# Kernel tuning notes

Hardware: AMD Instinct MI355X
Metric: run time of the kernel (lower is better)

The kernel has to match this reference:

```python
import jax, jax.numpy as jnp
import numpy as np

N = 100_000   # nodes
E = 1_600_000 # edges (avg degree 16)
D = 64        # in_channel == out_channel (residual requires equality)
EPS = 1e-5    # BatchNorm1d eps


def setup_inputs() -> dict:
    key = jax.random.key(0)
    ks = jax.random.split(key, 8)
    x = jax.random.normal(ks[0], (N, D), dtype=jnp.float32)
    adj_val = jax.random.uniform(ks[1], (E,), dtype=jnp.float32) * 0.25  # sparse poly_adj values
    W = jax.random.normal(ks[2], (D, D), dtype=jnp.float32) / np.sqrt(D)  # Linear weight [out,in]
    b = jnp.zeros((D,), dtype=jnp.float32)
    gamma = jnp.ones((D,), dtype=jnp.float32)
    beta = jnp.zeros((D,), dtype=jnp.float32)
    adj_row = jax.random.randint(ks[3], (E,), 0, N, dtype=jnp.int32)
    adj_col = jax.random.randint(ks[4], (E,), 0, N, dtype=jnp.int32)
    return {"x": x, "adj_val": adj_val, "W": W, "b": b,
            "gamma": gamma, "beta": beta, "adj_row": adj_row, "adj_col": adj_col}


def reference(x, adj_val, W, b, gamma, beta, adj_row, adj_col):
    # h = poly_adj @ x  (COO SpMM via gather + segment_sum)
    h = jax.ops.segment_sum(adj_val[:, None] * x[adj_col], adj_row, num_segments=N)
    # Linear
    h = h @ W.T + b
    # residual
    h = h + x
    # BatchNorm1d (training-mode batch stats, biased variance)
    mean = jnp.mean(h, axis=0)
    var = jnp.mean(jnp.square(h - mean), axis=0)
    h = (h - mean) * jax.lax.rsqrt(var + EPS) * gamma + beta
    # ReLU (dropout with p=0 is identity)
    h = jax.nn.relu(h)
    return h
```

## Files before the change

### kernel.cpp

```cpp
#include <hip/hip_runtime.h>

#define DCH 64
#define BN_EPS 1e-5f

#define SUPSH 12
#define NSUPMAX 32
#define CAPS 67584
#define CHA 2048
#define CHB 2048
#define CPS 33
#define FPS 128
#define CAPF 704
#define CITER 8
#define SITER 3

__device__ __forceinline__ unsigned bf16pair(float lo, float hi) {
    unsigned ul = (__float_as_uint(lo) + 0x8000u) >> 16;
    unsigned uh = (__float_as_uint(hi) + 0x8000u) & 0xffff0000u;
    return ul | uh;
}
__device__ __forceinline__ float bf_lo(unsigned u) { return __uint_as_float(u << 16); }
__device__ __forceinline__ float bf_hi(unsigned u) { return __uint_as_float(u & 0xffff0000u); }

__global__ __launch_bounds__(256) void gemm_bin(const float* __restrict__ x,
                                                const float* __restrict__ W,
                                                unsigned short* __restrict__ yb,
                                                const int* __restrict__ rows,
                                                const int* __restrict__ cols,
                                                const float* __restrict__ vals,
                                                int* __restrict__ cursA,
                                                int2* __restrict__ edgesA,
                                                int N, int E, int GB, int BB,
                                                int NSUP) {
    __shared__ __align__(16) char smem[51200];
    const int tid = threadIdx.x;
    const int role = blockIdx.x & 1;
    const int idx = blockIdx.x >> 1;

    if (role == 0) {
        if (idx >= GB) return;
        float* xs = (float*)smem;
        float* wt = (float*)(smem + 34816);
        const int blockRow = idx * 128;

#pragma unroll
        for (int jj = 0; jj < 4; ++jj) {
            int idx4 = tid * 16 + jj * 4;
            int o = idx4 >> 6, k = idx4 & 63;
            float4 w4 = *(const float4*)&W[idx4];
            wt[(k + 0) * 64 + o] = w4.x;
            wt[(k + 1) * 64 + o] = w4.y;
            wt[(k + 2) * 64 + o] = w4.z;
            wt[(k + 3) * 64 + o] = w4.w;
        }
#pragma unroll
        for (int jj = 0; jj < 8; ++jj) {
            int f4 = tid + 256 * jj;
            int rl = f4 >> 4, k4 = (f4 & 15) * 4;
            int row = blockRow + rl;
            float4 v = make_float4(0.f, 0.f, 0.f, 0.f);
            if (row < N) v = *(const float4*)&x[row * DCH + k4];
            *(float4*)&xs[rl * 68 + k4] = v;
        }
        __syncthreads();

        const int tc = tid & 7;
        const int tr = tid >> 3;
        const int dc = tc * 8;
        float acc[4][8];
#pragma unroll
        for (int i = 0; i < 4; ++i)
#pragma unroll
            for (int j = 0; j < 8; ++j) acc[i][j] = 0.f;

        for (int k4 = 0; k4 < 16; ++k4) {
            float4 xv[4];
#pragma unroll
            for (int i = 0; i < 4; ++i)
                xv[i] = *(const float4*)&xs[(tr + 32 * i) * 68 + k4 * 4];
#pragma unroll
            for (int kk = 0; kk < 4; ++kk) {
                int k = k4 * 4 + kk;
                float4 w0 = *(const float4*)&wt[k * 64 + dc];
                float4 w1 = *(const float4*)&wt[k * 64 + dc + 4];
#pragma unroll
                for (int i = 0; i < 4; ++i) {
                    float xvi = (kk == 0) ? xv[i].x : (kk == 1) ? xv[i].y
                               : (kk == 2) ? xv[i].z : xv[i].w;
                    acc[i][0] = fmaf(xvi, w0.x, acc[i][0]);
                    acc[i][1] = fmaf(xvi, w0.y, acc[i][1]);
                    acc[i][2] = fmaf(xvi, w0.z, acc[i][2]);
                    acc[i][3] = fmaf(xvi, w0.w, acc[i][3]);
                    acc[i][4] = fmaf(xvi, w1.x, acc[i][4]);
                    acc[i][5] = fmaf(xvi, w1.y, acc[i][5]);
                    acc[i][6] = fmaf(xvi, w1.z, acc[i][6]);
                    acc[i][7] = fmaf(xvi, w1.w, acc[i][7]);
                }
            }
        }
#pragma unroll
        for (int i = 0; i < 4; ++i) {
            int row = blockRow + tr + 32 * i;
            if (row < N) {
                uint4 p;
                p.x = bf16pair(acc[i][0], acc[i][1]);
                p.y = bf16pair(acc[i][2], acc[i][3]);
                p.z = bf16pair(acc[i][4], acc[i][5]);
                p.w = bf16pair(acc[i][6], acc[i][7]);
                *(uint4*)&yb[row * DCH + dc] = p;
            }
        }
    } else {
        if (idx >= BB) return;
        int2* stage = (int2*)smem;
        unsigned char* bOf = (unsigned char*)(smem + 16384);
        int* hist   = (int*)(smem + 18432);
        int* startB = (int*)(smem + 18560);
        int* gbase  = (int*)(smem + 18688);
        const int lane = tid & 63, wave = tid >> 6;
        const int base = idx * CHA;
        const int cnt = min(CHA, E - base);

        for (int i = tid; i < NSUPMAX; i += 256) hist[i] = 0;
        __syncthreads();

        int myr[CITER], mycol[CITER], myrank[CITER];
        float myv[CITER];
#pragma unroll
        for (int it = 0; it < CITER; ++it) {
            int k = tid + it * 256;
            if (k < cnt) {
                int r = rows[base + k];
                myr[it] = r;
                mycol[it] = cols[base + k];
                myv[it] = vals[base + k];
                myrank[it] = atomicAdd(&hist[r >> SUPSH], 1);
            }
        }
        __syncthreads();
        if (wave == 0) {
            int v = (lane < NSUP) ? hist[lane] : 0;
            int inc = v;
#pragma unroll
            for (int off = 1; off < 32; off <<= 1) {
                int u = __shfl_up(inc, off);
                if (lane >= off) inc += u;
            }
            if (lane < NSUP) {
                startB[lane] = inc - v;
                gbase[lane] = v ? atomicAdd(&cursA[lane], v) : 0;
            }
        }
        __syncthreads();
#pragma unroll
        for (int it = 0; it < CITER; ++it) {
            int k = tid + it * 256;
            if (k < cnt) {
                int key = myr[it] >> SUPSH;
                int pos = startB[key] + myrank[it];
                int2 pk;
                pk.x = mycol[it] | ((myr[it] & 4095) << 17);
                pk.y = __float_as_int(myv[it]);
                stage[pos] = pk;
                bOf[pos] = (unsigned char)key;
            }
        }
        __syncthreads();
#pragma unroll
        for (int it = 0; it < CITER; ++it) {
            int i = tid + it * 256;
            if (i < cnt) {
                int s = bOf[i];
                int rel = gbase[s] + (i - startB[s]);
                if (rel < CAPS) edgesA[s * CAPS + rel] = stage[i];
            }
        }
    }
}

__global__ __launch_bounds__(256) void bin_fine(const int2* __restrict__ edgesA,
                                                const int* __restrict__ cursA,
                                                int* __restrict__ cursB,
                                                int2* __restrict__ edgesB) {
    __shared__ int2 stage[CHB];
    __shared__ unsigned char bOf[CHB];
    __shared__ int hist[FPS], startB[FPS], gbase[FPS];
    const int tid = threadIdx.x, lane = tid & 63, wave = tid >> 6;
    const int s = blockIdx.x / CPS;
    const int c = blockIdx.x % CPS;
    const int base = s * CAPS + c * CHB;
    int fill = min(cursA[s], CAPS);
    int cnt = max(0, min(CHB, fill - c * CHB));

    for (int i = tid; i < FPS; i += 256) hist[i] = 0;
    __syncthreads();

    int2 mypk[CITER];
    int myrank[CITER];
#pragma unroll
    for (int it = 0; it < CITER; ++it) {
        int k = tid + it * 256;
        if (k < cnt) {
            int2 p = edgesA[base + k];
            mypk[it] = p;
            myrank[it] = atomicAdd(&hist[(p.x >> 22) & 127], 1);
        }
    }
    __syncthreads();
    if (wave == 0) {
        int v0 = hist[2 * lane], v1 = hist[2 * lane + 1];
        int p = v0 + v1;
        int inc = p;
#pragma unroll
        for (int off = 1; off < 64; off <<= 1) {
            int u = __shfl_up(inc, off);
            if (lane >= off) inc += u;
        }
        int b0 = inc - p;
        startB[2 * lane] = b0;
        startB[2 * lane + 1] = b0 + v0;
        gbase[2 * lane]     = v0 ? atomicAdd(&cursB[s * FPS + 2 * lane], v0) : 0;
        gbase[2 * lane + 1] = v1 ? atomicAdd(&cursB[s * FPS + 2 * lane + 1], v1) : 0;
    }
    __syncthreads();
#pragma unroll
    for (int it = 0; it < CITER; ++it) {
        int k = tid + it * 256;
        if (k < cnt) {
            int2 p = mypk[it];
            int key = (p.x >> 22) & 127;
            int pos = startB[key] + myrank[it];
            stage[pos] = p;
            bOf[pos] = (unsigned char)key;
        }
    }
    __syncthreads();
#pragma unroll
    for (int it = 0; it < CITER; ++it) {
        int i = tid + it * 256;
        if (i < cnt) {
            int f = bOf[i];
            int rel = gbase[f] + (i - startB[f]);
            if (rel < CAPF) edgesB[(size_t)(s * FPS + f) * CAPF + rel] = stage[i];
        }
    }
}

__global__ __launch_bounds__(256) void spmm_sorted(const unsigned short* __restrict__ yb,
                                                   const int* __restrict__ cursB,
                                                   const int2* __restrict__ edges,
                                                   const float* __restrict__ x,
                                                   const float* __restrict__ bias,
                                                   unsigned short* __restrict__ zb,
                                                   float* __restrict__ stats, int N) {
    __shared__ int2 cv[CAPF];
    __shared__ int hist[32];
    __shared__ int startE[33];
    __shared__ float rs[4][64];
    __shared__ float rs2[4][64];

    const int tid = threadIdx.x;
    const int b = blockIdx.x;
    const size_t beg = (size_t)b * CAPF;
    int cnt = min(cursB[b], CAPF);
    const int g = tid >> 3;
    const int q8 = tid & 7;
    const int wave = tid >> 6;
    const int lane = tid & 63;
    const int rowBase = b << 5;

    if (tid < 32) hist[tid] = 0;
    __syncthreads();

    int2 mypk[SITER];
    int myrank[SITER];
#pragma unroll
    for (int it = 0; it < SITER; ++it) {
        int k = tid + it * 256;
        if (k < cnt) {
            int2 p = edges[beg + k];
            mypk[it] = p;
            myrank[it] = atomicAdd(&hist[(p.x >> 17) & 31], 1);
        }
    }
    __syncthreads();
    if (wave == 0) {
        int v = (lane < 32) ? hist[lane] : 0;
        int inc = v;
#pragma unroll
        for (int off = 1; off < 32; off <<= 1) {
            int u = __shfl_up(inc, off);
            if (lane >= off) inc += u;
        }
        if (lane < 32) startE[lane] = inc - v;
        if (lane == 31) startE[32] = inc;
    }
    __syncthreads();
#pragma unroll
    for (int it = 0; it < SITER; ++it) {
        int k = tid + it * 256;
        if (k < cnt) {
            int2 p = mypk[it];
            int key = (p.x >> 17) & 31;
            int2 pc;
            pc.x = p.x & 0x1ffff;
            pc.y = p.y;
            cv[startE[key] + myrank[it]] = pc;
        }
    }
    __syncthreads();

    float bs[8];
    *(float4*)&bs[0] = *(const float4*)&bias[q8 * 8];
    *(float4*)&bs[4] = *(const float4*)&bias[q8 * 8 + 4];

    const int e0 = startE[g];
    const int e1 = startE[g + 1];
    float a[8];
#pragma unroll
    for (int i = 0; i < 8; ++i) a[i] = 0.f;

    for (int j = e0; j < e1; j += 8) {
        int cc[8];
        float vv[8];
#pragma unroll
        for (int u = 0; u < 8; ++u) {
            int idx = j + u;
            bool ok = idx < e1;
            int2 pc = cv[ok ? idx : e0];
            vv[u] = ok ? __int_as_float(pc.y) : 0.f;
            cc[u] = pc.x;
        }
        uint4 yq[8];
#pragma unroll
        for (int u = 0; u < 8; ++u)
            yq[u] = *(const uint4*)&yb[cc[u] * DCH + q8 * 8];
#pragma unroll
        for (int u = 0; u < 8; ++u) {
            a[0] = fmaf(vv[u], bf_lo(yq[u].x), a[0]);
            a[1] = fmaf(vv[u], bf_hi(yq[u].x), a[1]);
            a[2] = fmaf(vv[u], bf_lo(yq[u].y), a[2]);
            a[3] = fmaf(vv[u], bf_hi(yq[u].y), a[3]);
            a[4] = fmaf(vv[u], bf_lo(yq[u].z), a[4]);
            a[5] = fmaf(vv[u], bf_hi(yq[u].z), a[5]);
            a[6] = fmaf(vv[u], bf_lo(yq[u].w), a[6]);
            a[7] = fmaf(vv[u], bf_hi(yq[u].w), a[7]);
        }
    }

    float s[8], s2[8];
#pragma unroll
    for (int i = 0; i < 8; ++i) { s[i] = 0.f; s2[i] = 0.f; }

    {
        int r = rowBase + g;
        if (r < N) {
            float xv[8];
            *(float4*)&xv[0] = *(const float4*)&x[r * DCH + q8 * 8];
            *(float4*)&xv[4] = *(const float4*)&x[r * DCH + q8 * 8 + 4];
            float z[8];
#pragma unroll
            for (int i = 0; i < 8; ++i) {
                z[i] = a[i] + bs[i] + xv[i];
                s[i] += z[i];
                s2[i] = fmaf(z[i], z[i], s2[i]);
            }
            uint4 pz;
            pz.x = bf16pair(z[0], z[1]);
            pz.y = bf16pair(z[2], z[3]);
            pz.z = bf16pair(z[4], z[5]);
            pz.w = bf16pair(z[6], z[7]);
            *(uint4*)&zb[r * DCH + q8 * 8] = pz;
        }
    }

#pragma unroll
    for (int m = 8; m <= 32; m <<= 1) {
#pragma unroll
        for (int i = 0; i < 8; ++i) {
            s[i] += __shfl_xor(s[i], m);
            s2[i] += __shfl_xor(s2[i], m);
        }
    }
    if (lane < 8) {
        *(float4*)&rs[wave][q8 * 8]      = *(float4*)&s[0];
        *(float4*)&rs[wave][q8 * 8 + 4]  = *(float4*)&s[4];
        *(float4*)&rs2[wave][q8 * 8]     = *(float4*)&s2[0];
        *(float4*)&rs2[wave][q8 * 8 + 4] = *(float4*)&s2[4];
    }
    __syncthreads();
    if (tid < 64) {
        float ts  = rs[0][tid] + rs[1][tid] + rs[2][tid] + rs[3][tid];
        float ts2 = rs2[0][tid] + rs2[1][tid] + rs2[2][tid] + rs2[3][tid];
        float* st = stats + ((b & 7) << 7);
        atomicAdd(&st[tid], ts);
        atomicAdd(&st[64 + tid], ts2);
    }
}

__global__ __launch_bounds__(256) void bn_relu(const unsigned short* __restrict__ zb,
                                               float* __restrict__ out,
                                               const float* __restrict__ stats,
                                               const float* __restrict__ gamma,
                                               const float* __restrict__ beta,
                                               int ND8, float invN) {
    __shared__ float lsc[64], lsh[64];
    const int tid = threadIdx.x;
    if (tid < 64) {
        float s = 0.f, s2 = 0.f;
#pragma unroll
        for (int r = 0; r < 8; ++r) {
            s  += stats[r * 128 + tid];
            s2 += stats[r * 128 + 64 + tid];
        }
        float mean = s * invN;
        float var = s2 * invN - mean * mean;
        float sc = gamma[tid] * rsqrtf(var + BN_EPS);
        lsc[tid] = sc;
        lsh[tid] = beta[tid] - mean * sc;
    }
    __syncthreads();

    const int idx0 = blockIdx.x * 256 + tid;
    const int q8 = idx0 & 7;
    float sc[8], sh[8];
#pragma unroll
    for (int i = 0; i < 8; ++i) {
        sc[i] = lsc[q8 * 8 + i];
        sh[i] = lsh[q8 * 8 + i];
    }
    const int stride = gridDim.x * 256;
    for (int i = idx0; i < ND8; i += stride) {
        uint4 zq = *(const uint4*)&zb[i * 8];
        float z[8];
        z[0] = bf_lo(zq.x); z[1] = bf_hi(zq.x);
        z[2] = bf_lo(zq.y); z[3] = bf_hi(zq.y);
        z[4] = bf_lo(zq.z); z[5] = bf_hi(zq.z);
        z[6] = bf_lo(zq.w); z[7] = bf_hi(zq.w);
        float4 o0, o1;
        o0.x = fmaxf(fmaf(z[0], sc[0], sh[0]), 0.f);
        o0.y = fmaxf(fmaf(z[1], sc[1], sh[1]), 0.f);
        o0.z = fmaxf(fmaf(z[2], sc[2], sh[2]), 0.f);
        o0.w = fmaxf(fmaf(z[3], sc[3], sh[3]), 0.f);
        o1.x = fmaxf(fmaf(z[4], sc[4], sh[4]), 0.f);
        o1.y = fmaxf(fmaf(z[5], sc[5], sh[5]), 0.f);
        o1.z = fmaxf(fmaf(z[6], sc[6], sh[6]), 0.f);
        o1.w = fmaxf(fmaf(z[7], sc[7], sh[7]), 0.f);
        *(float4*)&out[i * 8] = o0;
        *(float4*)&out[i * 8 + 4] = o1;
    }
}

extern "C" void kernel_launch(void* const* d_in, const int* in_sizes, int n_in,
                              void* d_out, int out_size, void* d_ws, size_t ws_size,
                              hipStream_t stream) {
    const float* x       = (const float*)d_in[0];
    const float* adj_val = (const float*)d_in[1];
    const float* W       = (const float*)d_in[2];
    const float* b       = (const float*)d_in[3];
    const float* gamma   = (const float*)d_in[4];
    const float* beta    = (const float*)d_in[5];
    const int*   adj_row = (const int*)d_in[6];
    const int*   adj_col = (const int*)d_in[7];
    float* out = (float*)d_out;

    const int N  = in_sizes[0] / DCH;
    const int E  = in_sizes[1];
    const int ND = N * DCH;
    const int NSUP = (N + (1 << SUPSH) - 1) >> SUPSH;
    const int NFB  = NSUP * FPS;

    char* ws = (char*)d_ws;
    float* stats = (float*)ws;
    int* cursA   = (int*)(ws + 4096);
    int* cursB   = (int*)(ws + 4224);
    size_t off = 17024;
    unsigned short* yb = (unsigned short*)(ws + off); off += (size_t)ND * 2;
    off = (off + 127) & ~127ull;
    unsigned short* zb = (unsigned short*)(ws + off); off += (size_t)ND * 2;
    off = (off + 127) & ~127ull;
    int2* edgesA = (int2*)(ws + off);  off += (size_t)NSUP * CAPS * 8;
    int2* edgesB = (int2*)(ws + off);  off += (size_t)NFB * CAPF * 8;

    hipMemsetAsync(ws, 0, 17024, stream);

    const int GB = (N + 127) / 128;
    const int BB = (E + CHA - 1) / CHA;
    const int PAIRS = (GB > BB) ? GB : BB;

    gemm_bin<<<2 * PAIRS, 256, 0, stream>>>(x, W, yb, adj_row, adj_col, adj_val,
                                            cursA, edgesA, N, E, GB, BB, NSUP);
    bin_fine<<<NSUP * CPS, 256, 0, stream>>>(edgesA, cursA, cursB, edgesB);
    spmm_sorted<<<NFB, 256, 0, stream>>>(yb, cursB, edgesB, x, b, zb, stats, N);
    bn_relu<<<1024, 256, 0, stream>>>(zb, out, stats, gamma, beta, ND / 8,
                                      1.0f / (float)N);
}
```

Baseline: 176.4 us.

## Fuse fine binning, SpMM and BN-ReLU into one cooperative persistent kernel

Replaces the three tail launches (bin_fine, spmm_sorted, bn_relu) with a single cooperative kernel. It runs the binning tasks in a grid-stride loop, then does grid.sync, pulls SpMM row blocks through an atomic ticket counter, does another grid.sync, and finally applies BN+ReLU. The aim is to remove kernel launch gaps and inter-kernel drain and fill, and to balance the uneven SpMM blocks dynamically. In exchange it pays for grid-wide barriers and a persistent grid sized by occupancy, which may hold fewer resident waves than the separate launches did.

```diff
diff --git a/kernel.cpp b/kernel.cpp
--- a/kernel.cpp
+++ b/kernel.cpp
@@ -1,4 +1,7 @@
 #include <hip/hip_runtime.h>
+#include <hip/hip_cooperative_groups.h>
+
+namespace cg = cooperative_groups;
 
 #define DCH 64
 #define BN_EPS 1e-5f
@@ -178,276 +181,298 @@
     }
 }
 
-__global__ __launch_bounds__(256) void bin_fine(const int2* __restrict__ edgesA,
-                                                const int* __restrict__ cursA,
-                                                int* __restrict__ cursB,
-                                                int2* __restrict__ edgesB) {
-    __shared__ int2 stage[CHB];
-    __shared__ unsigned char bOf[CHB];
-    __shared__ int hist[FPS], startB[FPS], gbase[FPS];
-    const int tid = threadIdx.x, lane = tid & 63, wave = tid >> 6;
-    const int s = blockIdx.x / CPS;
-    const int c = blockIdx.x % CPS;
-    const int base = s * CAPS + c * CHB;
-    int fill = min(cursA[s], CAPS);
-    int cnt = max(0, min(CHB, fill - c * CHB));
-
-    for (int i = tid; i < FPS; i += 256) hist[i] = 0;
-    __syncthreads();
-
-    int2 mypk[CITER];
-    int myrank[CITER];
-#pragma unroll
-    for (int it = 0; it < CITER; ++it) {
-        int k = tid + it * 256;
-        if (k < cnt) {
-            int2 p = edgesA[base + k];
-            mypk[it] = p;
-            myrank[it] = atomicAdd(&hist[(p.x >> 22) & 127], 1);
+__global__ __launch_bounds__(256) void tail_fused(
+        const unsigned short* __restrict__ yb,
+        const int* __restrict__ cursA,
+        int* __restrict__ cursB,
+        const int2* __restrict__ edgesA,
+        int2* __restrict__ edgesB,
+        const float* __restrict__ x,
+        const float* __restrict__ bias,
+        unsigned short* __restrict__ zb,
+        float* __restrict__ stats,
+        const float* __restrict__ gamma,
+        const float* __restrict__ beta,
+        float* __restrict__ out,
+        int* __restrict__ ticket,
+        int N, int NSUP, int ND8, float invN) {
+    cg::grid_group grid = cg::this_grid();
+    __shared__ __align__(16) char smem[19968];
+    __shared__ int tsh;
+    const int tid = threadIdx.x;
+    const int lane = tid & 63, wave = tid >> 6;
+    const int G = gridDim.x;
+
+    {
+        int2* stage = (int2*)smem;
+        unsigned char* bOf = (unsigned char*)(smem + 16384);
+        int* hist   = (int*)(smem + 18432);
+        int* startB = (int*)(smem + 18944);
+        int* gbase  = (int*)(smem + 19456);
+        const int NTASK = NSUP * CPS;
+        for (int t = blockIdx.x; t < NTASK; t += G) {
+            const int s = t / CPS;
+            const int c = t % CPS;
+            const int base = s * CAPS + c * CHB;
+            int fill = min(cursA[s], CAPS);
+            int cnt = max(0, min(CHB, fill - c * CHB));
+
+            for (int i = tid; i < FPS; i += 256) hist[i] = 0;
+            __syncthreads();
+
+            int2 mypk[CITER];
+            int myrank[CITER];
+#pragma unroll
+            for (int it = 0; it < CITER; ++it) {
+                int k = tid + it * 256;
+                if (k < cnt) {
+                    int2 p = edgesA[base + k];
+                    mypk[it] = p;
+                    myrank[it] = atomicAdd(&hist[(p.x >> 22) & 127], 1);
+                }
+            }
+            __syncthreads();
+            if (wave == 0) {
+                int v0 = hist[2 * lane], v1 = hist[2 * lane + 1];
+                int p = v0 + v1;
+                int inc = p;
+#pragma unroll
+                for (int off = 1; off < 64; off <<= 1) {
+                    int u = __shfl_up(inc, off);
+                    if (lane >= off) inc += u;
+                }
+                int b0 = inc - p;
+                startB[2 * lane] = b0;
+                startB[2 * lane + 1] = b0 + v0;
+                gbase[2 * lane]     = v0 ? atomicAdd(&cursB[s * FPS + 2 * lane], v0) : 0;
+                gbase[2 * lane + 1] = v1 ? atomicAdd(&cursB[s * FPS + 2 * lane + 1], v1) : 0;
+            }
+            __syncthreads();
+#pragma unroll
+            for (int it = 0; it < CITER; ++it) {
+                int k = tid + it * 256;
+                if (k < cnt) {
+                    int2 p = mypk[it];
+                    int key = (p.x >> 22) & 127;
+                    int pos = startB[key] + myrank[it];
+                    stage[pos] = p;
+                    bOf[pos] = (unsigned char)key;
+                }
+            }
+            __syncthreads();
+#pragma unroll
+            for (int it = 0; it < CITER; ++it) {
+                int i = tid + it * 256;
+                if (i < cnt) {
+                    int f = bOf[i];
+                    int rel = gbase[f] + (i - startB[f]);
+                    if (rel < CAPF) edgesB[(size_t)(s * FPS + f) * CAPF + rel] = stage[i];
+                }
+            }
+            __syncthreads();
         }
     }
-    __syncthreads();
-    if (wave == 0) {
-        int v0 = hist[2 * lane], v1 = hist[2 * lane + 1];
-        int p = v0 + v1;
-        int inc = p;
-#pragma unroll
-        for (int off = 1; off < 64; off <<= 1) {
-            int u = __shfl_up(inc, off);
-            if (lane >= off) inc += u;
-        }
-        int b0 = inc - p;
-        startB[2 * lane] = b0;
-        startB[2 * lane + 1] = b0 + v0;
-        gbase[2 * lane]     = v0 ? atomicAdd(&cursB[s * FPS + 2 * lane], v0) : 0;
-        gbase[2 * lane + 1] = v1 ? atomicAdd(&cursB[s * FPS + 2 * lane + 1], v1) : 0;
+
+    grid.sync();
+
+    {
+        int2*  cv     = (int2*)smem;
+        int*   hist   = (int*)(smem + 5632);
+        int*   startE = (int*)(smem + 5760);
+        float* rs     = (float*)(smem + 5920);
+        float* rs2    = (float*)(smem + 6944);
+        const int g  = tid >> 3;
+        const int q8 = tid & 7;
+        const int NFB = NSUP * FPS;
+
+        float bs[8];
+        *(float4*)&bs[0] = *(const float4*)&bias[q8 * 8];
+        *(float4*)&bs[4] = *(const float4*)&bias[q8 * 8 + 4];
+
+        for (;;) {
+            if (tid == 0) tsh = atomicAdd(ticket, 1);
+            __syncthreads();
+            const int b = tsh;
+            if (b >= NFB) break;
+            const size_t beg = (size_t)b * CAPF;
+            int cnt = min(cursB[b], CAPF);
+            const int rowBase = b << 5;
+
+            if (tid < 32) hist[tid] = 0;
+            __syncthreads();
+
+            int2 mypk[SITER];
+            int myrank[SITER];
+#pragma unroll
+            for (int it = 0; it < SITER; ++it) {
+                int k = tid + it * 256;
+                if (k < cnt) {
+                    int2 p = edgesB[beg + k];
+                    mypk[it] = p;
+                    myrank[it] = atomicAdd(&hist[(p.x >> 17) & 31], 1);
+                }
+            }
+            __syncthreads();
+            if (wave == 0) {
+                int v = (lane < 32) ? hist[lane] : 0;
+                int inc = v;
+#pragma unroll
+                for (int off = 1; off < 32; off <<= 1) {
+                    int u = __shfl_up(inc, off);
+                    if (lane >= off) inc += u;
+                }
+                if (lane < 32) startE[lane] = inc - v;
+                if (lane == 31) startE[32] = inc;
+            }
+            __syncthreads();
+#pragma unroll
+            for (int it = 0; it < SITER; ++it) {
+                int k = tid + it * 256;
+                if (k < cnt) {
+                    int2 p = mypk[it];
+                    int key = (p.x >> 17) & 31;
+                    int2 pc;
+                    pc.x = p.x & 0x1ffff;
+                    pc.y = p.y;
+                    cv[startE[key] + myrank[it]] = pc;
+                }
+            }
+            __syncthreads();
+
+            const int e0 = startE[g];
+            const int e1 = startE[g + 1];
+            float a[8];
+#pragma unroll
+            for (int i = 0; i < 8; ++i) a[i] = 0.f;
+
+            for (int j = e0; j < e1; j += 8) {
+                int cc[8];
+                float vv[8];
+#pragma unroll
+                for (int u = 0; u < 8; ++u) {
+                    int idx = j + u;
+                    bool ok = idx < e1;
+                    int2 pc = cv[ok ? idx : e0];
+                    vv[u] = ok ? __int_as_float(pc.y) : 0.f;
+                    cc[u] = pc.x;
+                }
+                uint4 yq[8];
+#pragma unroll
+                for (int u = 0; u < 8; ++u)
+                    yq[u] = *(const uint4*)&yb[cc[u] * DCH + q8 * 8];
+#pragma unroll
+                for (int u = 0; u < 8; ++u) {
+                    a[0] = fmaf(vv[u], bf_lo(yq[u].x), a[0]);
+                    a[1] = fmaf(vv[u], bf_hi(yq[u].x), a[1]);
+                    a[2] = fmaf(vv[u], bf_lo(yq[u].y), a[2]);
+                    a[3] = fmaf(vv[u], bf_hi(yq[u].y), a[3]);
+                    a[4] = fmaf(vv[u], bf_lo(yq[u].z), a[4]);
+                    a[5] = fmaf(vv[u], bf_hi(yq[u].z), a[5]);
+                    a[6] = fmaf(vv[u], bf_lo(yq[u].w), a[6]);
+                    a[7] = fmaf(vv[u], bf_hi(yq[u].w), a[7]);
+                }
+            }
+
+            float s[8], s2[8];
+#pragma unroll
+            for (int i = 0; i < 8; ++i) { s[i] = 0.f; s2[i] = 0.f; }
+
+            {
+                int r = rowBase + g;
+                if (r < N) {
+                    float xv[8];
+                    *(float4*)&xv[0] = *(const float4*)&x[r * DCH + q8 * 8];
+                    *(float4*)&xv[4] = *(const float4*)&x[r * DCH + q8 * 8 + 4];
+                    float z[8];
+#pragma unroll
+                    for (int i = 0; i < 8; ++i) {
+                        z[i] = a[i] + bs[i] + xv[i];
+                        s[i] += z[i];
+                        s2[i] = fmaf(z[i], z[i], s2[i]);
+                    }
+                    uint4 pz;
+                    pz.x = bf16pair(z[0], z[1]);
+                    pz.y = bf16pair(z[2], z[3]);
+                    pz.z = bf16pair(z[4], z[5]);
+                    pz.w = bf16pair(z[6], z[7]);
+                    *(uint4*)&zb[r * DCH + q8 * 8] = pz;
+                }
+            }
+
+#pragma unroll
+            for (int m = 8; m <= 32; m <<= 1) {
+#pragma unroll
+                for (int i = 0; i < 8; ++i) {
+                    s[i] += __shfl_xor(s[i], m);
+                    s2[i] += __shfl_xor(s2[i], m);
+                }
+            }
+            if (lane < 8) {
+                *(float4*)&rs[wave * 64 + q8 * 8]      = *(float4*)&s[0];
+                *(float4*)&rs[wave * 64 + q8 * 8 + 4]  = *(float4*)&s[4];
+                *(float4*)&rs2[wave * 64 + q8 * 8]     = *(float4*)&s2[0];
+                *(float4*)&rs2[wave * 64 + q8 * 8 + 4] = *(float4*)&s2[4];
+            }
+            __syncthreads();
+            if (tid < 64) {
+                float ts  = rs[0 * 64 + tid] + rs[1 * 64 + tid] + rs[2 * 64 + tid] + rs[3 * 64 + tid];
+                float ts2 = rs2[0 * 64 + tid] + rs2[1 * 64 + tid] + rs2[2 * 64 + tid] + rs2[3 * 64 + tid];
+                float* st = stats + ((b & 7) << 7);
+                atomicAdd(&st[tid], ts);
+                atomicAdd(&st[64 + tid], ts2);
+            }
+            __syncthreads();
+        }
     }
-    __syncthreads();
-#pragma unroll
-    for (int it = 0; it < CITER; ++it) {
-        int k = tid + it * 256;
-        if (k < cnt) {
-            int2 p = mypk[it];
-            int key = (p.x >> 22) & 127;
-            int pos = startB[key] + myrank[it];
-            stage[pos] = p;
-            bOf[pos] = (unsigned char)key;
-        }
-    }
-    __syncthreads();
-#pragma unroll
-    for (int it = 0; it < CITER; ++it) {
-        int i = tid + it * 256;
-        if (i < cnt) {
-            int f = bOf[i];
-            int rel = gbase[f] + (i - startB[f]);
-            if (rel < CAPF) edgesB[(size_t)(s * FPS + f) * CAPF + rel] = stage[i];
-        }
-    }
-}
-
-__global__ __launch_bounds__(256) void spmm_sorted(const unsigned short* __restrict__ yb,
-                                                   const int* __restrict__ cursB,
-                                                   const int2* __restrict__ edges,
-                                                   const float* __restrict__ x,
-                                                   const float* __restrict__ bias,
-                                                   unsigned short* __restrict__ zb,
-                                                   float* __restrict__ stats, int N) {
-    __shared__ int2 cv[CAPF];
-    __shared__ int hist[32];
-    __shared__ int startE[33];
-    __shared__ float rs[4][64];
-    __shared__ float rs2[4][64];
-
-    const int tid = threadIdx.x;
-    const int b = blockIdx.x;
-    const size_t beg = (size_t)b * CAPF;
-    int cnt = min(cursB[b], CAPF);
-    const int g = tid >> 3;
-    const int q8 = tid & 7;
-    const int wave = tid >> 6;
-    const int lane = tid & 63;
-    const int rowBase = b << 5;
-
-    if (tid < 32) hist[tid] = 0;
-    __syncthreads();
-
-    int2 mypk[SITER];
-    int myrank[SITER];
-#pragma unroll
-    for (int it = 0; it < SITER; ++it) {
-        int k = tid + it * 256;
-        if (k < cnt) {
-            int2 p = edges[beg + k];
-            mypk[it] = p;
-            myrank[it] = atomicAdd(&hist[(p.x >> 17) & 31], 1);
-        }
-    }
-    __syncthreads();
-    if (wave == 0) {
-        int v = (lane < 32) ? hist[lane] : 0;
-        int inc = v;
-#pragma unroll
-        for (int off = 1; off < 32; off <<= 1) {
-            int u = __shfl_up(inc, off);
-            if (lane >= off) inc += u;
-        }
-        if (lane < 32) startE[lane] = inc - v;
-        if (lane == 31) startE[32] = inc;
-    }
-    __syncthreads();
-#pragma unroll
-    for (int it = 0; it < SITER; ++it) {
-        int k = tid + it * 256;
-        if (k < cnt) {
-            int2 p = mypk[it];
-            int key = (p.x >> 17) & 31;
-            int2 pc;
-            pc.x = p.x & 0x1ffff;
-            pc.y = p.y;
-            cv[startE[key] + myrank[it]] = pc;
-        }
-    }
-    __syncthreads();
-
-    float bs[8];
-    *(float4*)&bs[0] = *(const float4*)&bias[q8 * 8];
-    *(float4*)&bs[4] = *(const float4*)&bias[q8 * 8 + 4];
-
-    const int e0 = startE[g];
-    const int e1 = startE[g + 1];
-    float a[8];
-#pragma unroll
-    for (int i = 0; i < 8; ++i) a[i] = 0.f;
-
-    for (int j = e0; j < e1; j += 8) {
-        int cc[8];
-        float vv[8];
-#pragma unroll
-        for (int u = 0; u < 8; ++u) {
-            int idx = j + u;
-            bool ok = idx < e1;
-            int2 pc = cv[ok ? idx : e0];
-            vv[u] = ok ? __int_as_float(pc.y) : 0.f;
-            cc[u] = pc.x;
-        }
-        uint4 yq[8];
-#pragma unroll
-        for (int u = 0; u < 8; ++u)
-            yq[u] = *(const uint4*)&yb[cc[u] * DCH + q8 * 8];
-#pragma unroll
-        for (int u = 0; u < 8; ++u) {
-            a[0] = fmaf(vv[u], bf_lo(yq[u].x), a[0]);
-            a[1] = fmaf(vv[u], bf_hi(yq[u].x), a[1]);
-            a[2] = fmaf(vv[u], bf_lo(yq[u].y), a[2]);
-            a[3] = fmaf(vv[u], bf_hi(yq[u].y), a[3]);
-            a[4] = fmaf(vv[u], bf_lo(yq[u].z), a[4]);
-            a[5] = fmaf(vv[u], bf_hi(yq[u].z), a[5]);
-            a[6] = fmaf(vv[u], bf_lo(yq[u].w), a[6]);
-            a[7] = fmaf(vv[u], bf_hi(yq[u].w), a[7]);
-        }
-    }
-
-    float s[8], s2[8];
-#pragma unroll
-    for (int i = 0; i < 8; ++i) { s[i] = 0.f; s2[i] = 0.f; }
+
+    grid.sync();
 
     {
-        int r = rowBase + g;
-        if (r < N) {
-            float xv[8];
-            *(float4*)&xv[0] = *(const float4*)&x[r * DCH + q8 * 8];
-            *(float4*)&xv[4] = *(const float4*)&x[r * DCH + q8 * 8 + 4];
+        float* lsc = (float*)smem;
+        float* lsh = (float*)(smem + 256);
+        if (tid < 64) {
+            float s = 0.f, s2 = 0.f;
+#pragma unroll
+            for (int r = 0; r < 8; ++r) {
+                s  += stats[r * 128 + tid];
+                s2 += stats[r * 128 + 64 + tid];
+            }
+            float mean = s * invN;
+            float var = s2 * invN - mean * mean;
+            float sc = gamma[tid] * rsqrtf(var + BN_EPS);
+            lsc[tid] = sc;
+            lsh[tid] = beta[tid] - mean * sc;
+        }
+        __syncthreads();
+
+        const int idx0 = blockIdx.x * 256 + tid;
+        const int q8 = idx0 & 7;
+        float sc[8], sh[8];
+#pragma unroll
+        for (int i = 0; i < 8; ++i) {
+            sc[i] = lsc[q8 * 8 + i];
+            sh[i] = lsh[q8 * 8 + i];
+        }
+        const int stride = G * 256;
+        for (int i = idx0; i < ND8; i += stride) {
+            uint4 zq = *(const uint4*)&zb[i * 8];
             float z[8];
-#pragma unroll
-            for (int i = 0; i < 8; ++i) {
-                z[i] = a[i] + bs[i] + xv[i];
-                s[i] += z[i];
-                s2[i] = fmaf(z[i], z[i], s2[i]);
-            }
-            uint4 pz;
-            pz.x = bf16pair(z[0], z[1]);
-            pz.y = bf16pair(z[2], z[3]);
-            pz.z = bf16pair(z[4], z[5]);
-            pz.w = bf16pair(z[6], z[7]);
-            *(uint4*)&zb[r * DCH + q8 * 8] = pz;
-        }
-    }
-
-#pragma unroll
-    for (int m = 8; m <= 32; m <<= 1) {
-#pragma unroll
-        for (int i = 0; i < 8; ++i) {
-            s[i] += __shfl_xor(s[i], m);
-            s2[i] += __shfl_xor(s2[i], m);
-        }
-    }
-    if (lane < 8) {
-        *(float4*)&rs[wave][q8 * 8]      = *(float4*)&s[0];
-        *(float4*)&rs[wave][q8 * 8 + 4]  = *(float4*)&s[4];
-        *(float4*)&rs2[wave][q8 * 8]     = *(float4*)&s2[0];
-        *(float4*)&rs2[wave][q8 * 8 + 4] = *(float4*)&s2[4];
-    }
-    __syncthreads();
-    if (tid < 64) {
-        float ts  = rs[0][tid] + rs[1][tid] + rs[2][tid] + rs[3][tid];
-        float ts2 = rs2[0][tid] + rs2[1][tid] + rs2[2][tid] + rs2[3][tid];
-        float* st = stats + ((b & 7) << 7);
-        atomicAdd(&st[tid], ts);
-        atomicAdd(&st[64 + tid], ts2);
-    }
-}
-
-__global__ __launch_bounds__(256) void bn_relu(const unsigned short* __restrict__ zb,
-                                               float* __restrict__ out,
-                                               const float* __restrict__ stats,
-                                               const float* __restrict__ gamma,
-                                               const float* __restrict__ beta,
-                                               int ND8, float invN) {
-    __shared__ float lsc[64], lsh[64];
-    const int tid = threadIdx.x;
-    if (tid < 64) {
-        float s = 0.f, s2 = 0.f;
-#pragma unroll
-        for (int r = 0; r < 8; ++r) {
-            s  += stats[r * 128 + tid];
-            s2 += stats[r * 128 + 64 + tid];
-        }
-        float mean = s * invN;
-        float var = s2 * invN - mean * mean;
-        float sc = gamma[tid] * rsqrtf(var + BN_EPS);
-        lsc[tid] = sc;
-        lsh[tid] = beta[tid] - mean * sc;
-    }
-    __syncthreads();
-
-    const int idx0 = blockIdx.x * 256 + tid;
-    const int q8 = idx0 & 7;
-    float sc[8], sh[8];
-#pragma unroll
-    for (int i = 0; i < 8; ++i) {
-        sc[i] = lsc[q8 * 8 + i];
-        sh[i] = lsh[q8 * 8 + i];
-    }
-    const int stride = gridDim.x * 256;
-    for (int i = idx0; i < ND8; i += stride) {
-        uint4 zq = *(const uint4*)&zb[i * 8];
-        float z[8];
-        z[0] = bf_lo(zq.x); z[1] = bf_hi(zq.x);
-        z[2] = bf_lo(zq.y); z[3] = bf_hi(zq.y);
-        z[4] = bf_lo(zq.z); z[5] = bf_hi(zq.z);
-        z[6] = bf_lo(zq.w); z[7] = bf_hi(zq.w);
-        float4 o0, o1;
-        o0.x = fmaxf(fmaf(z[0], sc[0], sh[0]), 0.f);
-        o0.y = fmaxf(fmaf(z[1], sc[1], sh[1]), 0.f);
-        o0.z = fmaxf(fmaf(z[2], sc[2], sh[2]), 0.f);
-        o0.w = fmaxf(fmaf(z[3], sc[3], sh[3]), 0.f);
-        o1.x = fmaxf(fmaf(z[4], sc[4], sh[4]), 0.f);
-        o1.y = fmaxf(fmaf(z[5], sc[5], sh[5]), 0.f);
-        o1.z = fmaxf(fmaf(z[6], sc[6], sh[6]), 0.f);
-        o1.w = fmaxf(fmaf(z[7], sc[7], sh[7]), 0.f);
-        *(float4*)&out[i * 8] = o0;
-        *(float4*)&out[i * 8 + 4] = o1;
+            z[0] = bf_lo(zq.x); z[1] = bf_hi(zq.x);
+            z[2] = bf_lo(zq.y); z[3] = bf_hi(zq.y);
+            z[4] = bf_lo(zq.z); z[5] = bf_hi(zq.z);
+            z[6] = bf_lo(zq.w); z[7] = bf_hi(zq.w);
+            float4 o0, o1;
+            o0.x = fmaxf(fmaf(z[0], sc[0], sh[0]), 0.f);
+            o0.y = fmaxf(fmaf(z[1], sc[1], sh[1]), 0.f);
+            o0.z = fmaxf(fmaf(z[2], sc[2], sh[2]), 0.f);
+            o0.w = fmaxf(fmaf(z[3], sc[3], sh[3]), 0.f);
+            o1.x = fmaxf(fmaf(z[4], sc[4], sh[4]), 0.f);
+            o1.y = fmaxf(fmaf(z[5], sc[5], sh[5]), 0.f);
+            o1.z = fmaxf(fmaf(z[6], sc[6], sh[6]), 0.f);
+            o1.w = fmaxf(fmaf(z[7], sc[7], sh[7]), 0.f);
+            *(float4*)&out[i * 8] = o0;
+            *(float4*)&out[i * 8 + 4] = o1;
+        }
     }
 }
 
@@ -474,7 +499,8 @@
     float* stats = (float*)ws;
     int* cursA   = (int*)(ws + 4096);
     int* cursB   = (int*)(ws + 4224);
-    size_t off = 17024;
+    int* ticket  = (int*)(ws + 17024);
+    size_t off = 17152;
     unsigned short* yb = (unsigned short*)(ws + off); off += (size_t)ND * 2;
     off = (off + 127) & ~127ull;
     unsigned short* zb = (unsigned short*)(ws + off); off += (size_t)ND * 2;
@@ -482,7 +508,7 @@
     int2* edgesA = (int2*)(ws + off);  off += (size_t)NSUP * CAPS * 8;
     int2* edgesB = (int2*)(ws + off);  off += (size_t)NFB * CAPF * 8;
 
-    hipMemsetAsync(ws, 0, 17024, stream);
+    hipMemsetAsync(ws, 0, 17152, stream);
 
     const int GB = (N + 127) / 128;
     const int BB = (E + CHA - 1) / CHA;
@@ -490,8 +516,28 @@
 
     gemm_bin<<<2 * PAIRS, 256, 0, stream>>>(x, W, yb, adj_row, adj_col, adj_val,
                                             cursA, edgesA, N, E, GB, BB, NSUP);
-    bin_fine<<<NSUP * CPS, 256, 0, stream>>>(edgesA, cursA, cursB, edgesB);
-    spmm_sorted<<<NFB, 256, 0, stream>>>(yb, cursB, edgesB, x, b, zb, stats, N);
-    bn_relu<<<1024, 256, 0, stream>>>(zb, out, stats, gamma, beta, ND / 8,
-                                      1.0f / (float)N);
+
+    static int g_coop_grid = 0;
+    if (g_coop_grid == 0) {
+        int nb = 0;
+        hipOccupancyMaxActiveBlocksPerMultiprocessor(&nb, tail_fused, 256, 0);
+        if (nb < 1) nb = 1;
+        hipDeviceProp_t prop;
+        int dev = 0;
+        hipGetDevice(&dev);
+        hipGetDeviceProperties(&prop, dev);
+        int cap = nb * prop.multiProcessorCount;
+        if (cap < 256) cap = 256;
+        g_coop_grid = cap < 2048 ? cap : 2048;
+    }
+
+    int N_ = N, NSUP_ = NSUP, ND8_ = ND / 8;
+    float invN_ = 1.0f / (float)N;
+    void* args[] = { (void*)&yb, (void*)&cursA, (void*)&cursB, (void*)&edgesA,
+                     (void*)&edgesB, (void*)&x, (void*)&b, (void*)&zb,
+                     (void*)&stats, (void*)&gamma, (void*)&beta, (void*)&out,
+                     (void*)&ticket, (void*)&N_, (void*)&NSUP_, (void*)&ND8_,
+                     (void*)&invN_ };
+    hipLaunchCooperativeKernel((const void*)tail_fused, dim3(g_coop_grid),
+                               dim3(256), args, 0, stream);
 }
```

Result: slower. 328.9 us (+86.4%).

## Replace per-block row sort with LDS tile scatter via shared atomics

Applied to the files above, without the earlier changes.

The SpMM block no longer counting-sorts its edges by local row into shared memory. Each thread now gathers y rows for edges in arbitrary order and accumulates into a padded 32x64 LDS float tile with shared-memory atomicAdd. This drops the histogram, scan and scatter passes and their barriers, and gives every thread an equal share of edges regardless of row degree. In exchange it issues eight LDS atomics per edge per thread and makes the floating-point summation order nondeterministic.

```diff
diff --git a/kernel.cpp b/kernel.cpp
--- a/kernel.cpp
+++ b/kernel.cpp
@@ -12,7 +12,7 @@
 #define FPS 128
 #define CAPF 704
 #define CITER 8
-#define SITER 3
+#define TS 69
 
 __device__ __forceinline__ unsigned bf16pair(float lo, float hi) {
     unsigned ul = (__float_as_uint(lo) + 0x8000u) >> 16;
@@ -246,16 +246,14 @@
     }
 }
 
-__global__ __launch_bounds__(256) void spmm_sorted(const unsigned short* __restrict__ yb,
-                                                   const int* __restrict__ cursB,
-                                                   const int2* __restrict__ edges,
-                                                   const float* __restrict__ x,
-                                                   const float* __restrict__ bias,
-                                                   unsigned short* __restrict__ zb,
-                                                   float* __restrict__ stats, int N) {
-    __shared__ int2 cv[CAPF];
-    __shared__ int hist[32];
-    __shared__ int startE[33];
+__global__ __launch_bounds__(256) void spmm_tile(const unsigned short* __restrict__ yb,
+                                                 const int* __restrict__ cursB,
+                                                 const int2* __restrict__ edges,
+                                                 const float* __restrict__ x,
+                                                 const float* __restrict__ bias,
+                                                 unsigned short* __restrict__ zb,
+                                                 float* __restrict__ stats, int N) {
+    __shared__ float tile[32 * TS];
     __shared__ float rs[4][64];
     __shared__ float rs2[4][64];
 
@@ -269,84 +267,39 @@
     const int lane = tid & 63;
     const int rowBase = b << 5;
 
-    if (tid < 32) hist[tid] = 0;
-    __syncthreads();
-
-    int2 mypk[SITER];
-    int myrank[SITER];
-#pragma unroll
-    for (int it = 0; it < SITER; ++it) {
-        int k = tid + it * 256;
-        if (k < cnt) {
-            int2 p = edges[beg + k];
-            mypk[it] = p;
-            myrank[it] = atomicAdd(&hist[(p.x >> 17) & 31], 1);
-        }
-    }
-    __syncthreads();
-    if (wave == 0) {
-        int v = (lane < 32) ? hist[lane] : 0;
-        int inc = v;
-#pragma unroll
-        for (int off = 1; off < 32; off <<= 1) {
-            int u = __shfl_up(inc, off);
-            if (lane >= off) inc += u;
-        }
-        if (lane < 32) startE[lane] = inc - v;
-        if (lane == 31) startE[32] = inc;
-    }
-    __syncthreads();
-#pragma unroll
-    for (int it = 0; it < SITER; ++it) {
-        int k = tid + it * 256;
-        if (k < cnt) {
-            int2 p = mypk[it];
-            int key = (p.x >> 17) & 31;
-            int2 pc;
-            pc.x = p.x & 0x1ffff;
-            pc.y = p.y;
-            cv[startE[key] + myrank[it]] = pc;
-        }
-    }
-    __syncthreads();
-
-    float bs[8];
-    *(float4*)&bs[0] = *(const float4*)&bias[q8 * 8];
-    *(float4*)&bs[4] = *(const float4*)&bias[q8 * 8 + 4];
-
-    const int e0 = startE[g];
-    const int e1 = startE[g + 1];
-    float a[8];
-#pragma unroll
-    for (int i = 0; i < 8; ++i) a[i] = 0.f;
-
-    for (int j = e0; j < e1; j += 8) {
-        int cc[8];
-        float vv[8];
+    for (int i = tid; i < 32 * TS; i += 256) tile[i] = 0.f;
+    __syncthreads();
+
+    for (int base = 0; base < cnt; base += 256) {
+        int rr[8];
+        float mv[8];
+        uint4 yq[8];
 #pragma unroll
         for (int u = 0; u < 8; ++u) {
-            int idx = j + u;
-            bool ok = idx < e1;
-            int2 pc = cv[ok ? idx : e0];
-            vv[u] = ok ? __int_as_float(pc.y) : 0.f;
-            cc[u] = pc.x;
-        }
-        uint4 yq[8];
-#pragma unroll
-        for (int u = 0; u < 8; ++u)
-            yq[u] = *(const uint4*)&yb[cc[u] * DCH + q8 * 8];
+            int e = base + g + 32 * u;
+            bool ok = e < cnt;
+            int2 p = edges[beg + (ok ? e : 0)];
+            rr[u] = (p.x >> 17) & 31;
+            mv[u] = ok ? __int_as_float(p.y) : 0.f;
+            int cc = p.x & 0x1ffff;
+            yq[u] = *(const uint4*)&yb[cc * DCH + q8 * 8];
+        }
 #pragma unroll
         for (int u = 0; u < 8; ++u) {
-            a[0] = fmaf(vv[u], bf_lo(yq[u].x), a[0]);
-            a[1] = fmaf(vv[u], bf_hi(yq[u].x), a[1]);
-            a[2] = fmaf(vv[u], bf_lo(yq[u].y), a[2]);
-            a[3] = fmaf(vv[u], bf_hi(yq[u].y), a[3]);
-            a[4] = fmaf(vv[u], bf_lo(yq[u].z), a[4]);
-            a[5] = fmaf(vv[u], bf_hi(yq[u].z), a[5]);
-            a[6] = fmaf(vv[u], bf_lo(yq[u].w), a[6]);
-            a[7] = fmaf(vv[u], bf_hi(yq[u].w), a[7]);
-        }
-    }
+            if (base + g + 32 * u < cnt) {
+                float* tr = &tile[rr[u] * TS + q8 * 8];
+                atomicAdd(&tr[0], mv[u] * bf_lo(yq[u].x));
+                atomicAdd(&tr[1], mv[u] * bf_hi(yq[u].x));
+                atomicAdd(&tr[2], mv[u] * bf_lo(yq[u].y));
+                atomicAdd(&tr[3], mv[u] * bf_hi(yq[u].y));
+                atomicAdd(&tr[4], mv[u] * bf_lo(yq[u].z));
+                atomicAdd(&tr[5], mv[u] * bf_hi(yq[u].z));
+                atomicAdd(&tr[6], mv[u] * bf_lo(yq[u].w));
+                atomicAdd(&tr[7], mv[u] * bf_hi(yq[u].w));
+            }
+        }
+    }
+    __syncthreads();
 
     float s[8], s2[8];
 #pragma unroll
@@ -355,13 +308,15 @@
     {
         int r = rowBase + g;
         if (r < N) {
-            float xv[8];
+            float bs[8], xv[8];
+            *(float4*)&bs[0] = *(const float4*)&bias[q8 * 8];
+            *(float4*)&bs[4] = *(const float4*)&bias[q8 * 8 + 4];
             *(float4*)&xv[0] = *(const float4*)&x[r * DCH + q8 * 8];
             *(float4*)&xv[4] = *(const float4*)&x[r * DCH + q8 * 8 + 4];
             float z[8];
 #pragma unroll
             for (int i = 0; i < 8; ++i) {
-                z[i] = a[i] + bs[i] + xv[i];
+                z[i] = tile[g * TS + q8 * 8 + i] + bs[i] + xv[i];
                 s[i] += z[i];
                 s2[i] = fmaf(z[i], z[i], s2[i]);
             }
@@ -491,7 +446,7 @@
     gemm_bin<<<2 * PAIRS, 256, 0, stream>>>(x, W, yb, adj_row, adj_col, adj_val,
                                             cursA, edgesA, N, E, GB, BB, NSUP);
     bin_fine<<<NSUP * CPS, 256, 0, stream>>>(edgesA, cursA, cursB, edgesB);
-    spmm_sorted<<<NFB, 256, 0, stream>>>(yb, cursB, edgesB, x, b, zb, stats, N);
+    spmm_tile<<<NFB, 256, 0, stream>>>(yb, cursB, edgesB, x, b, zb, stats, N);
     bn_relu<<<1024, 256, 0, stream>>>(zb, out, stats, gamma, beta, ND / 8,
                                       1.0f / (float)N);
 }
```

New measurement: 699.1 us. 296% more time.

## Balance SpMM edge work evenly across row groups using shared-memory atomic accumulation

Applied to the files above, without the earlier changes.

Each 8-thread group now takes an equal contiguous slice of the block's row-sorted edges instead of one row's variable-length segment. Partial sums are flushed with LDS float atomics into a padded 32x69 shared tile whenever the row changes, and the epilogue reads the tile. This targets load imbalance from uneven row degrees within a block. The cost is a tile clear, extra atomics and a barrier, and the floating-point summation order now varies between runs.

```diff
diff --git a/kernel.cpp b/kernel.cpp
--- a/kernel.cpp
+++ b/kernel.cpp
@@ -13,6 +13,7 @@
 #define CAPF 704
 #define CITER 8
 #define SITER 3
+#define TS 69
 
 __device__ __forceinline__ unsigned bf16pair(float lo, float hi) {
     unsigned ul = (__float_as_uint(lo) + 0x8000u) >> 16;
@@ -254,6 +255,7 @@
                                                    unsigned short* __restrict__ zb,
                                                    float* __restrict__ stats, int N) {
     __shared__ int2 cv[CAPF];
+    __shared__ float tile[32 * TS];
     __shared__ int hist[32];
     __shared__ int startE[33];
     __shared__ float rs[4][64];
@@ -270,6 +272,7 @@
     const int rowBase = b << 5;
 
     if (tid < 32) hist[tid] = 0;
+    for (int i = tid; i < 32 * TS; i += 256) tile[i] = 0.f;
     __syncthreads();
 
     int2 mypk[SITER];
@@ -302,51 +305,64 @@
         if (k < cnt) {
             int2 p = mypk[it];
             int key = (p.x >> 17) & 31;
-            int2 pc;
-            pc.x = p.x & 0x1ffff;
-            pc.y = p.y;
-            cv[startE[key] + myrank[it]] = pc;
-        }
-    }
-    __syncthreads();
-
-    float bs[8];
-    *(float4*)&bs[0] = *(const float4*)&bias[q8 * 8];
-    *(float4*)&bs[4] = *(const float4*)&bias[q8 * 8 + 4];
-
-    const int e0 = startE[g];
-    const int e1 = startE[g + 1];
+            cv[startE[key] + myrank[it]] = p;
+        }
+    }
+    __syncthreads();
+
+    const int e_lo = (cnt * g) >> 5;
+    const int e_hi = (cnt * (g + 1)) >> 5;
     float a[8];
 #pragma unroll
     for (int i = 0; i < 8; ++i) a[i] = 0.f;
-
-    for (int j = e0; j < e1; j += 8) {
-        int cc[8];
+    int cur = -1;
+
+#define FLUSH()                                                     \
+    if (cur >= 0) {                                                 \
+        float* tr = &tile[cur * TS + q8 * 8];                       \
+        atomicAdd(&tr[0], a[0]); atomicAdd(&tr[1], a[1]);           \
+        atomicAdd(&tr[2], a[2]); atomicAdd(&tr[3], a[3]);           \
+        atomicAdd(&tr[4], a[4]); atomicAdd(&tr[5], a[5]);           \
+        atomicAdd(&tr[6], a[6]); atomicAdd(&tr[7], a[7]);           \
+    }
+
+    for (int j = e_lo; j < e_hi; j += 8) {
+        int rr[8];
         float vv[8];
+        uint4 yq[8];
 #pragma unroll
         for (int u = 0; u < 8; ++u) {
             int idx = j + u;
-            bool ok = idx < e1;
-            int2 pc = cv[ok ? idx : e0];
-            vv[u] = ok ? __int_as_float(pc.y) : 0.f;
-            cc[u] = pc.x;
-        }
-        uint4 yq[8];
-#pragma unroll
-        for (int u = 0; u < 8; ++u)
-            yq[u] = *(const uint4*)&yb[cc[u] * DCH + q8 * 8];
+            bool ok = idx < e_hi;
+            int2 p = cv[ok ? idx : e_lo];
+            rr[u] = (p.x >> 17) & 31;
+            vv[u] = ok ? __int_as_float(p.y) : 0.f;
+            int cc = p.x & 0x1ffff;
+            yq[u] = *(const uint4*)&yb[cc * DCH + q8 * 8];
+        }
 #pragma unroll
         for (int u = 0; u < 8; ++u) {
-            a[0] = fmaf(vv[u], bf_lo(yq[u].x), a[0]);
-            a[1] = fmaf(vv[u], bf_hi(yq[u].x), a[1]);
-            a[2] = fmaf(vv[u], bf_lo(yq[u].y), a[2]);
-            a[3] = fmaf(vv[u], bf_hi(yq[u].y), a[3]);
-            a[4] = fmaf(vv[u], bf_lo(yq[u].z), a[4]);
-            a[5] = fmaf(vv[u], bf_hi(yq[u].z), a[5]);
-            a[6] = fmaf(vv[u], bf_lo(yq[u].w), a[6]);
-            a[7] = fmaf(vv[u], bf_hi(yq[u].w), a[7]);
-        }
-    }
+            if (j + u < e_hi) {
+                if (rr[u] != cur) {
+                    FLUSH();
+                    cur = rr[u];
+#pragma unroll
+                    for (int i = 0; i < 8; ++i) a[i] = 0.f;
+                }
+                a[0] = fmaf(vv[u], bf_lo(yq[u].x), a[0]);
+                a[1] = fmaf(vv[u], bf_hi(yq[u].x), a[1]);
+                a[2] = fmaf(vv[u], bf_lo(yq[u].y), a[2]);
+                a[3] = fmaf(vv[u], bf_hi(yq[u].y), a[3]);
+                a[4] = fmaf(vv[u], bf_lo(yq[u].z), a[4]);
+                a[5] = fmaf(vv[u], bf_hi(yq[u].z), a[5]);
+                a[6] = fmaf(vv[u], bf_lo(yq[u].w), a[6]);
+                a[7] = fmaf(vv[u], bf_hi(yq[u].w), a[7]);
+            }
+        }
+    }
+    FLUSH();
+#undef FLUSH
+    __syncthreads();
 
     float s[8], s2[8];
 #pragma unroll
@@ -355,13 +371,15 @@
     {
         int r = rowBase + g;
         if (r < N) {
-            float xv[8];
+            float bs[8], xv[8];
+            *(float4*)&bs[0] = *(const float4*)&bias[q8 * 8];
+            *(float4*)&bs[4] = *(const float4*)&bias[q8 * 8 + 4];
             *(float4*)&xv[0] = *(const float4*)&x[r * DCH + q8 * 8];
             *(float4*)&xv[4] = *(const float4*)&x[r * DCH + q8 * 8 + 4];
             float z[8];
 #pragma unroll
             for (int i = 0; i < 8; ++i) {
-                z[i] = a[i] + bs[i] + xv[i];
+                z[i] = tile[g * TS + q8 * 8 + i] + bs[i] + xv[i];
                 s[i] += z[i];
                 s2[i] = fmaf(z[i], z[i], s2[i]);
             }
```

Result: slower. 220.7 us (+25.1%).
